# Kernel optimization log

Measured on AMD Instinct MI355X. Metric: run time of the kernel, lower is better.

## Reference

```python
import jax, jax.numpy as jnp
import numpy as np

K = 1024
H = 16

def setup_inputs() -> dict:
    key = jax.random.key(0)
    ks = jax.random.split(key, 6)
    s = 1.0 / np.sqrt(K)
    return {
        "x": jax.random.normal(ks[0], (2, 2048, K), dtype=jnp.float32),
        "Wq": jax.random.uniform(ks[1], (K, K), jnp.float32, -s, s),
        "Wk": jax.random.uniform(ks[2], (K, K), jnp.float32, -s, s),
        "Wv": jax.random.uniform(ks[3], (K, K), jnp.float32, -s, s),
        "Wu": jax.random.uniform(ks[4], (K, K), jnp.float32, -s, s),
        "bu": jax.random.uniform(ks[5], (K,), jnp.float32, -s, s),
    }

def reference(x, Wq, Wk, Wv, Wu, bu):
    b, t, k = x.shape
    hd = k // H  # head dim = 64
    scale = jnp.asarray(k, x.dtype) ** 0.25  # Bloem-style: scale q and k each by k^(1/4)
    # nn.Linear(bias=False): y = x @ W.T
    q = (jnp.einsum('btk,ok->bto', x, Wq) / scale).reshape(b, t, H, hd)
    kk = (jnp.einsum('btk,ok->bto', x, Wk) / scale).reshape(b, t, H, hd)
    v = jnp.einsum('btk,ok->bto', x, Wv).reshape(b, t, H, hd)
    dot = jnp.einsum('bthd,bshd->bhts', q, kk)  # [b,h,t,t]
    att = jax.nn.softmax(dot, axis=-1)
    out = jnp.einsum('bhts,bshd->bthd', att, v).reshape(b, t, k)
    return jnp.einsum('btk,ok->bto', out, Wu) + bu
```

## Files before the change

### kernel.cpp

```cpp
#include <hip/hip_runtime.h>

typedef __bf16 bf16;
typedef bf16  bf16x8 __attribute__((ext_vector_type(8)));
typedef bf16  bf16x4 __attribute__((ext_vector_type(4)));
typedef float f32x4  __attribute__((ext_vector_type(4)));

#define MFMA16(a, b, c) __builtin_amdgcn_mfma_f32_16x16x32_bf16((a), (b), (c), 0, 0, 0)
#define AS1 __attribute__((address_space(1)))
#define AS3 __attribute__((address_space(3)))

__device__ __forceinline__ void gld_lds16(const bf16* g, bf16* l) {
    __builtin_amdgcn_global_load_lds((AS1 void*)(g), (AS3 void*)(l), 16, 0, 0);
}


__global__ __launch_bounds__(256) void cvt_x(const float* __restrict__ src, bf16* __restrict__ dst) {
    int idx = (blockIdx.x * 256 + threadIdx.x) * 4;
    float4 v = *(const float4*)(src + idx);
    bf16x4 o;
    o[0] = (bf16)v.x; o[1] = (bf16)v.y; o[2] = (bf16)v.z; o[3] = (bf16)v.w;
    *(bf16x4*)(dst + idx) = o;
}

__global__ __launch_bounds__(256) void cvt_weights(const float* __restrict__ Wq, const float* __restrict__ Wk,
                                                   const float* __restrict__ Wv, const float* __restrict__ Wu,
                                                   bf16* oq, bf16* ok, bf16* ov, bf16* ou,
                                                   float sq, float sk) {
    const float* src; bf16* dst; float sc;
    switch (blockIdx.y) {
        case 0:  src = Wq; dst = oq; sc = sq;   break;
        case 1:  src = Wk; dst = ok; sc = sk;   break;
        case 2:  src = Wv; dst = ov; sc = 1.0f; break;
        default: src = Wu; dst = ou; sc = 1.0f; break;
    }
    int idx = (blockIdx.x * 256 + threadIdx.x) * 4;
    float4 v = *(const float4*)(src + idx);
    bf16x4 o;
    o[0] = (bf16)(v.x * sc); o[1] = (bf16)(v.y * sc);
    o[2] = (bf16)(v.z * sc); o[3] = (bf16)(v.w * sc);
    *(bf16x4*)(dst + idx) = o;
}

__device__ __forceinline__ void gemm_core(const bf16* __restrict__ A, const bf16* __restrict__ B,
                                          int mBase, int nBase, bf16* As, bf16* Bs,
                                          f32x4 acc[4][4]) {
    const int tid = threadIdx.x;
    const int wave = tid >> 6, lane = tid & 63;
    const int g = lane >> 4, lr = lane & 15;
    const int wm = (wave & 1) << 6, wn = (wave >> 1) << 6;
    const int q = lane >> 2;
    const int cswz = ((lane & 3) ^ ((lane >> 3) & 3)) << 3;
    const int pcs  = (g ^ ((lr >> 1) & 3)) << 3;

    const int rb0 = wave << 4, rb1 = rb0 + 64;
    const bf16* a0 = A + (size_t)(mBase + rb0 + q) * 1024 + cswz;
    const bf16* a1 = A + (size_t)(mBase + rb1 + q) * 1024 + cswz;
    const bf16* b0 = B + (size_t)(nBase + rb0 + q) * 1024 + cswz;
    const bf16* b1 = B + (size_t)(nBase + rb1 + q) * 1024 + cswz;

    for (int k0 = 0; k0 < 1024; k0 += 32) {
        __syncthreads();
        gld_lds16(a0 + k0, As + rb0 * 32);
        gld_lds16(a1 + k0, As + rb1 * 32);
        gld_lds16(b0 + k0, Bs + rb0 * 32);
        gld_lds16(b1 + k0, Bs + rb1 * 32);
        __syncthreads();

        bf16x8 af[4], bfr[4];
#pragma unroll
        for (int i = 0; i < 4; i++)
            af[i] = *(const bf16x8*)&As[(wm + (i << 4) + lr) * 32 + pcs];
#pragma unroll
        for (int j = 0; j < 4; j++)
            bfr[j] = *(const bf16x8*)&Bs[(wn + (j << 4) + lr) * 32 + pcs];
#pragma unroll
        for (int i = 0; i < 4; i++)
#pragma unroll
            for (int j = 0; j < 4; j++)
                acc[i][j] = MFMA16(af[i], bfr[j], acc[i][j]);
    }
}

__global__ __launch_bounds__(256) void gemm_qkv(const bf16* __restrict__ A,
                                                const bf16* __restrict__ Wq, const bf16* __restrict__ Wk,
                                                const bf16* __restrict__ Wv,
                                                bf16* __restrict__ Qo, bf16* __restrict__ Ko,
                                                bf16* __restrict__ Vto) {
    __shared__ bf16 As[128 * 32];
    __shared__ bf16 Bs[128 * 32];
    const int tid = threadIdx.x;
    const int wave = tid >> 6, lane = tid & 63;
    const int g = lane >> 4, lr = lane & 15;
    const int wm = (wave & 1) << 6, wn = (wave >> 1) << 6;
    const int z = blockIdx.z;

    const bf16 *Ap, *Bp;
    int mBase, nBase;
    if (z == 2) { Ap = Wv; Bp = A;            mBase = blockIdx.x * 128; nBase = blockIdx.y * 128; }
    else        { Ap = A;  Bp = z ? Wk : Wq;  mBase = blockIdx.y * 128; nBase = blockIdx.x * 128; }

    f32x4 acc[4][4] = {};
    gemm_core(Ap, Bp, mBase, nBase, As, Bs, acc);

#pragma unroll
    for (int i = 0; i < 4; i++)
#pragma unroll
        for (int j = 0; j < 4; j++)
#pragma unroll
            for (int r = 0; r < 4; r++) {
                int m = mBase + wm + (i << 4) + (g << 2) + r;
                int n = nBase + wn + (j << 4) + lr;
                bf16 v = (bf16)acc[i][j][r];
                if (z == 2) {
                    int h = m >> 6, d = m & 63, b = n >> 11, t = n & 2047;
                    Vto[((size_t)(((b << 4) + h) << 6) + d) * 2048 + t] = v;
                } else {
                    int b = m >> 11, t = m & 2047, h = n >> 6, d = n & 63;
                    bf16* dst = (z == 0) ? Qo : Ko;
                    dst[(((size_t)((b << 4) + h) * 2048 + t) << 6) + d] = v;
                }
            }
}

__global__ __launch_bounds__(256) void gemm_out(const bf16* __restrict__ A, const bf16* __restrict__ B,
                                                const float* __restrict__ bias, float* __restrict__ out) {
    __shared__ bf16 As[128 * 32];
    __shared__ bf16 Bs[128 * 32];
    const int tid = threadIdx.x;
    const int wave = tid >> 6, lane = tid & 63;
    const int g = lane >> 4, lr = lane & 15;
    const int wm = (wave & 1) << 6, wn = (wave >> 1) << 6;
    const int mBase = blockIdx.y * 128, nBase = blockIdx.x * 128;

    f32x4 acc[4][4] = {};
    gemm_core(A, B, mBase, nBase, As, Bs, acc);

#pragma unroll
    for (int i = 0; i < 4; i++)
#pragma unroll
        for (int j = 0; j < 4; j++) {
            int n = nBase + wn + (j << 4) + lr;
            float bv = bias[n];
#pragma unroll
            for (int r = 0; r < 4; r++) {
                int m = mBase + wm + (i << 4) + (g << 2) + r;
                out[((size_t)m << 10) + n] = acc[i][j][r] + bv;
            }
        }
}

__global__ __launch_bounds__(256) void attn(const bf16* __restrict__ Q, const bf16* __restrict__ Kt,
                                            const bf16* __restrict__ Vt, bf16* __restrict__ O) {
    __shared__ bf16 Qs[2][128][32];
    __shared__ bf16 Ks[2][128][32];
    __shared__ bf16 Vs[4][64][32];
    bf16 (*Ps)[32][32] = (bf16(*)[32][32]) & Qs[0][0][0];

    const int tid = threadIdx.x;
    const int wave = tid >> 6, lane = tid & 63;
    const int g = lane >> 4, lr = lane & 15;
    const int q = lane >> 2;
    const int cswz = ((lane & 3) ^ ((lane >> 3) & 3)) << 3;
    const int pcs  = (g ^ ((lr >> 1) & 3)) << 3;
    const int pw0 = ((((g >> 1))     ^ ((lr >> 1) & 3)) << 3) + ((g & 1) << 2);
    const int pw1 = (((2 + (g >> 1)) ^ ((lr >> 1) & 3)) << 3) + ((g & 1) << 2);

    const int bh = blockIdx.y;
    const int qBase = blockIdx.x << 7;

    const bf16* Qg = Q + ((size_t)bh * 2048 + qBase) * 64;
    const bf16* Kg = Kt + (size_t)bh * 2048 * 64;
    const bf16* Vg = Vt + (size_t)bh * 64 * 2048;

#pragma unroll
    for (int i = 0; i < 4; i++) {
        int bi = (wave << 2) + i;
        int p = bi >> 3, rb = (bi & 7) << 4;
        gld_lds16(Qg + (rb + q) * 64 + (p << 5) + cswz, &Qs[p][rb][0]);
    }
    __syncthreads();

    bf16x8 qf[2][2];
#pragma unroll
    for (int ks = 0; ks < 2; ks++)
#pragma unroll
        for (int tt = 0; tt < 2; tt++)
            qf[ks][tt] = *(const bf16x8*)&Qs[ks][(wave << 5) + (tt << 4) + lr][pcs];

    f32x4 oacc[2][4] = {};
    float lsum[2] = {0.f, 0.f};

    for (int s0 = 0; s0 < 2048; s0 += 128) {
        __syncthreads();
#pragma unroll
        for (int i = 0; i < 4; i++) {
            int bi = (wave << 2) + i;
            {
                int p = bi >> 3, rb = (bi & 7) << 4;
                gld_lds16(Kg + (size_t)(s0 + rb + q) * 64 + (p << 5) + cswz, &Ks[p][rb][0]);
            }
            {
                int p = bi >> 2, rb = (bi & 3) << 4;
                gld_lds16(Vg + (size_t)(rb + q) * 2048 + s0 + (p << 5) + cswz, &Vs[p][rb][0]);
            }
        }
        __syncthreads();

#pragma unroll
        for (int ks2 = 0; ks2 < 4; ks2++) {
            f32x4 sacc[2][2] = {};
#pragma unroll
            for (int isub = 0; isub < 2; isub++) {
                int is = (ks2 << 1) + isub;
#pragma unroll
                for (int ks = 0; ks < 2; ks++) {
                    bf16x8 kf = *(const bf16x8*)&Ks[ks][(is << 4) + lr][pcs];
                    sacc[isub][0] = MFMA16(kf, qf[ks][0], sacc[isub][0]);
                    sacc[isub][1] = MFMA16(kf, qf[ks][1], sacc[isub][1]);
                }
            }
#pragma unroll
            for (int isub = 0; isub < 2; isub++)
#pragma unroll
                for (int tt = 0; tt < 2; tt++) {
                    f32x4 s = sacc[isub][tt];
                    float e0 = __builtin_amdgcn_exp2f(s[0]);
                    float e1 = __builtin_amdgcn_exp2f(s[1]);
                    float e2 = __builtin_amdgcn_exp2f(s[2]);
                    float e3 = __builtin_amdgcn_exp2f(s[3]);
                    lsum[tt] += (e0 + e1) + (e2 + e3);
                    bf16x4 pb;
                    pb[0] = (bf16)e0; pb[1] = (bf16)e1; pb[2] = (bf16)e2; pb[3] = (bf16)e3;
                    *(bf16x4*)&Ps[wave][(tt << 4) + lr][isub ? pw1 : pw0] = pb;
                }
            bf16x8 pf0 = *(const bf16x8*)&Ps[wave][lr][pcs];
            bf16x8 pf1 = *(const bf16x8*)&Ps[wave][16 + lr][pcs];
#pragma unroll
            for (int jd = 0; jd < 4; jd++) {
                bf16x8 vf = *(const bf16x8*)&Vs[ks2][(jd << 4) + lr][pcs];
                oacc[0][jd] = MFMA16(pf0, vf, oacc[0][jd]);
                oacc[1][jd] = MFMA16(pf1, vf, oacc[1][jd]);
            }
        }
    }

#pragma unroll
    for (int tt = 0; tt < 2; tt++) {
        lsum[tt] += __shfl_xor(lsum[tt], 16, 64);
        lsum[tt] += __shfl_xor(lsum[tt], 32, 64);
    }
    float linv[2][4];
#pragma unroll
    for (int tt = 0; tt < 2; tt++)
#pragma unroll
        for (int r = 0; r < 4; r++)
            linv[tt][r] = 1.0f / __shfl(lsum[tt], (g << 2) + r, 64);

    const int b = bh >> 4, h = bh & 15;
#pragma unroll
    for (int tt = 0; tt < 2; tt++)
#pragma unroll
        for (int jd = 0; jd < 4; jd++)
#pragma unroll
            for (int r = 0; r < 4; r++) {
                int t = qBase + (wave << 5) + (tt << 4) + (g << 2) + r;
                int col = (h << 6) + (jd << 4) + lr;
                O[(((size_t)(b * 2048 + t)) << 10) + col] = (bf16)(oacc[tt][jd][r] * linv[tt][r]);
            }
}

extern "C" void kernel_launch(void* const* d_in, const int* in_sizes, int n_in,
                              void* d_out, int out_size, void* d_ws, size_t ws_size,
                              hipStream_t stream) {
    const float* x  = (const float*)d_in[0];
    const float* Wq = (const float*)d_in[1];
    const float* Wk = (const float*)d_in[2];
    const float* Wv = (const float*)d_in[3];
    const float* Wu = (const float*)d_in[4];
    const float* bu = (const float*)d_in[5];
    float* out = (float*)d_out;

    char* ws = (char*)d_ws;
    bf16* xbf  = (bf16*)(ws);
    bf16* wqbf = (bf16*)(ws + ((size_t)8  << 20));
    bf16* wkbf = (bf16*)(ws + ((size_t)10 << 20));
    bf16* wvbf = (bf16*)(ws + ((size_t)12 << 20));
    bf16* wubf = (bf16*)(ws + ((size_t)14 << 20));
    bf16* Qb   = (bf16*)(ws + ((size_t)16 << 20));
    bf16* Kb   = (bf16*)(ws + ((size_t)24 << 20));
    bf16* Vtb  = (bf16*)(ws + ((size_t)32 << 20));
    bf16* attnO = xbf;

    const float iscale_k = 0.17677669529663687f;
    const float iscale_q = 0.25503540109f;

    cvt_x<<<4096, 256, 0, stream>>>(x, xbf);
    cvt_weights<<<dim3(1024, 4), 256, 0, stream>>>(Wq, Wk, Wv, Wu, wqbf, wkbf, wvbf, wubf,
                                                   iscale_q, iscale_k);

    gemm_qkv<<<dim3(8, 32, 3), 256, 0, stream>>>(xbf, wqbf, wkbf, wvbf, Qb, Kb, Vtb);
    attn<<<dim3(16, 32), 256, 0, stream>>>(Qb, Kb, Vtb, attnO);
    gemm_out<<<dim3(8, 32), 256, 0, stream>>>(attnO, wubf, bu, out);
}
```

Baseline: 200.4 us.

## Merge conversion kernels, double GEMM K-step, compute softmax row sums via MFMA

The x and weight conversion kernels are merged into one launch, saving one kernel launch. The GEMM core now loads 64-wide K tiles into two 32-wide LDS slabs per sync, which halves the number of barriers per K loop. In attention, the softmax denominator is accumulated by an extra MFMA against a vector of ones instead of scalar adds and cross-lane shuffles. That adds two MFMAs per step and sums the rounded bf16 probabilities, so the normalisation may differ slightly from the fp32 sums.

```diff
diff --git a/kernel.cpp b/kernel.cpp
--- a/kernel.cpp
+++ b/kernel.cpp
@@ -14,26 +14,24 @@
 }
 
 
-__global__ __launch_bounds__(256) void cvt_x(const float* __restrict__ src, bf16* __restrict__ dst) {
-    int idx = (blockIdx.x * 256 + threadIdx.x) * 4;
-    float4 v = *(const float4*)(src + idx);
-    bf16x4 o;
-    o[0] = (bf16)v.x; o[1] = (bf16)v.y; o[2] = (bf16)v.z; o[3] = (bf16)v.w;
-    *(bf16x4*)(dst + idx) = o;
-}
-
-__global__ __launch_bounds__(256) void cvt_weights(const float* __restrict__ Wq, const float* __restrict__ Wk,
-                                                   const float* __restrict__ Wv, const float* __restrict__ Wu,
-                                                   bf16* oq, bf16* ok, bf16* ov, bf16* ou,
-                                                   float sq, float sk) {
-    const float* src; bf16* dst; float sc;
-    switch (blockIdx.y) {
-        case 0:  src = Wq; dst = oq; sc = sq;   break;
-        case 1:  src = Wk; dst = ok; sc = sk;   break;
-        case 2:  src = Wv; dst = ov; sc = 1.0f; break;
-        default: src = Wu; dst = ou; sc = 1.0f; break;
+__global__ __launch_bounds__(256) void cvt_all(const float* __restrict__ x,
+                                               const float* __restrict__ Wq, const float* __restrict__ Wk,
+                                               const float* __restrict__ Wv, const float* __restrict__ Wu,
+                                               bf16* ox, bf16* oq, bf16* ok, bf16* ov, bf16* ou,
+                                               float sq, float sk) {
+    int bid = blockIdx.x;
+    const float* src; bf16* dst; float sc; int base;
+    if (bid < 4096) { src = x; dst = ox; sc = 1.0f; base = bid; }
+    else {
+        int w = (bid - 4096) >> 10; base = (bid - 4096) & 1023;
+        switch (w) {
+            case 0:  src = Wq; dst = oq; sc = sq;   break;
+            case 1:  src = Wk; dst = ok; sc = sk;   break;
+            case 2:  src = Wv; dst = ov; sc = 1.0f; break;
+            default: src = Wu; dst = ou; sc = 1.0f; break;
+        }
     }
-    int idx = (blockIdx.x * 256 + threadIdx.x) * 4;
+    int idx = (base * 256 + threadIdx.x) * 4;
     float4 v = *(const float4*)(src + idx);
     bf16x4 o;
     o[0] = (bf16)(v.x * sc); o[1] = (bf16)(v.y * sc);
@@ -42,7 +40,8 @@
 }
 
 __device__ __forceinline__ void gemm_core(const bf16* __restrict__ A, const bf16* __restrict__ B,
-                                          int mBase, int nBase, bf16* As, bf16* Bs,
+                                          int mBase, int nBase,
+                                          bf16 (*As)[128][32], bf16 (*Bs)[128][32],
                                           f32x4 acc[4][4]) {
     const int tid = threadIdx.x;
     const int wave = tid >> 6, lane = tid & 63;
@@ -52,32 +51,35 @@
     const int cswz = ((lane & 3) ^ ((lane >> 3) & 3)) << 3;
     const int pcs  = (g ^ ((lr >> 1) & 3)) << 3;
 
-    const int rb0 = wave << 4, rb1 = rb0 + 64;
-    const bf16* a0 = A + (size_t)(mBase + rb0 + q) * 1024 + cswz;
-    const bf16* a1 = A + (size_t)(mBase + rb1 + q) * 1024 + cswz;
-    const bf16* b0 = B + (size_t)(nBase + rb0 + q) * 1024 + cswz;
-    const bf16* b1 = B + (size_t)(nBase + rb1 + q) * 1024 + cswz;
-
-    for (int k0 = 0; k0 < 1024; k0 += 32) {
+    const int bi0 = wave << 2;
+
+    for (int k0 = 0; k0 < 1024; k0 += 64) {
         __syncthreads();
-        gld_lds16(a0 + k0, As + rb0 * 32);
-        gld_lds16(a1 + k0, As + rb1 * 32);
-        gld_lds16(b0 + k0, Bs + rb0 * 32);
-        gld_lds16(b1 + k0, Bs + rb1 * 32);
+#pragma unroll
+        for (int i = 0; i < 4; i++) {
+            int bi = bi0 + i;
+            int p = bi >> 3, rb = (bi & 7) << 4;
+            int kof = k0 + (p << 5) + cswz;
+            gld_lds16(A + (size_t)(mBase + rb + q) * 1024 + kof, &As[p][rb][0]);
+            gld_lds16(B + (size_t)(nBase + rb + q) * 1024 + kof, &Bs[p][rb][0]);
+        }
         __syncthreads();
 
-        bf16x8 af[4], bfr[4];
-#pragma unroll
-        for (int i = 0; i < 4; i++)
-            af[i] = *(const bf16x8*)&As[(wm + (i << 4) + lr) * 32 + pcs];
-#pragma unroll
-        for (int j = 0; j < 4; j++)
-            bfr[j] = *(const bf16x8*)&Bs[(wn + (j << 4) + lr) * 32 + pcs];
-#pragma unroll
-        for (int i = 0; i < 4; i++)
+#pragma unroll
+        for (int ks = 0; ks < 2; ks++) {
+            bf16x8 af[4], bfr[4];
+#pragma unroll
+            for (int i = 0; i < 4; i++)
+                af[i] = *(const bf16x8*)&As[ks][wm + (i << 4) + lr][pcs];
 #pragma unroll
             for (int j = 0; j < 4; j++)
-                acc[i][j] = MFMA16(af[i], bfr[j], acc[i][j]);
+                bfr[j] = *(const bf16x8*)&Bs[ks][wn + (j << 4) + lr][pcs];
+#pragma unroll
+            for (int i = 0; i < 4; i++)
+#pragma unroll
+                for (int j = 0; j < 4; j++)
+                    acc[i][j] = MFMA16(af[i], bfr[j], acc[i][j]);
+        }
     }
 }
 
@@ -86,8 +88,8 @@
                                                 const bf16* __restrict__ Wv,
                                                 bf16* __restrict__ Qo, bf16* __restrict__ Ko,
                                                 bf16* __restrict__ Vto) {
-    __shared__ bf16 As[128 * 32];
-    __shared__ bf16 Bs[128 * 32];
+    __shared__ bf16 As[2][128][32];
+    __shared__ bf16 Bs[2][128][32];
     const int tid = threadIdx.x;
     const int wave = tid >> 6, lane = tid & 63;
     const int g = lane >> 4, lr = lane & 15;
@@ -124,8 +126,8 @@
 
 __global__ __launch_bounds__(256) void gemm_out(const bf16* __restrict__ A, const bf16* __restrict__ B,
                                                 const float* __restrict__ bias, float* __restrict__ out) {
-    __shared__ bf16 As[128 * 32];
-    __shared__ bf16 Bs[128 * 32];
+    __shared__ bf16 As[2][128][32];
+    __shared__ bf16 Bs[2][128][32];
     const int tid = threadIdx.x;
     const int wave = tid >> 6, lane = tid & 63;
     const int g = lane >> 4, lr = lane & 15;
@@ -187,8 +189,12 @@
         for (int tt = 0; tt < 2; tt++)
             qf[ks][tt] = *(const bf16x8*)&Qs[ks][(wave << 5) + (tt << 4) + lr][pcs];
 
+    bf16x8 ones;
+#pragma unroll
+    for (int i = 0; i < 8; i++) ones[i] = (bf16)1.0f;
+
     f32x4 oacc[2][4] = {};
-    float lsum[2] = {0.f, 0.f};
+    f32x4 oaccL[2] = {};
 
     for (int s0 = 0; s0 < 2048; s0 += 128) {
         __syncthreads();
@@ -224,13 +230,11 @@
 #pragma unroll
                 for (int tt = 0; tt < 2; tt++) {
                     f32x4 s = sacc[isub][tt];
-                    float e0 = __builtin_amdgcn_exp2f(s[0]);
-                    float e1 = __builtin_amdgcn_exp2f(s[1]);
-                    float e2 = __builtin_amdgcn_exp2f(s[2]);
-                    float e3 = __builtin_amdgcn_exp2f(s[3]);
-                    lsum[tt] += (e0 + e1) + (e2 + e3);
                     bf16x4 pb;
-                    pb[0] = (bf16)e0; pb[1] = (bf16)e1; pb[2] = (bf16)e2; pb[3] = (bf16)e3;
+                    pb[0] = (bf16)__builtin_amdgcn_exp2f(s[0]);
+                    pb[1] = (bf16)__builtin_amdgcn_exp2f(s[1]);
+                    pb[2] = (bf16)__builtin_amdgcn_exp2f(s[2]);
+                    pb[3] = (bf16)__builtin_amdgcn_exp2f(s[3]);
                     *(bf16x4*)&Ps[wave][(tt << 4) + lr][isub ? pw1 : pw0] = pb;
                 }
             bf16x8 pf0 = *(const bf16x8*)&Ps[wave][lr][pcs];
@@ -241,20 +245,17 @@
                 oacc[0][jd] = MFMA16(pf0, vf, oacc[0][jd]);
                 oacc[1][jd] = MFMA16(pf1, vf, oacc[1][jd]);
             }
+            oaccL[0] = MFMA16(pf0, ones, oaccL[0]);
+            oaccL[1] = MFMA16(pf1, ones, oaccL[1]);
         }
     }
 
-#pragma unroll
-    for (int tt = 0; tt < 2; tt++) {
-        lsum[tt] += __shfl_xor(lsum[tt], 16, 64);
-        lsum[tt] += __shfl_xor(lsum[tt], 32, 64);
-    }
     float linv[2][4];
 #pragma unroll
     for (int tt = 0; tt < 2; tt++)
 #pragma unroll
         for (int r = 0; r < 4; r++)
-            linv[tt][r] = 1.0f / __shfl(lsum[tt], (g << 2) + r, 64);
+            linv[tt][r] = 1.0f / oaccL[tt][r];
 
     const int b = bh >> 4, h = bh & 15;
 #pragma unroll
@@ -294,9 +295,8 @@
     const float iscale_k = 0.17677669529663687f;
     const float iscale_q = 0.25503540109f;
 
-    cvt_x<<<4096, 256, 0, stream>>>(x, xbf);
-    cvt_weights<<<dim3(1024, 4), 256, 0, stream>>>(Wq, Wk, Wv, Wu, wqbf, wkbf, wvbf, wubf,
-                                                   iscale_q, iscale_k);
+    cvt_all<<<8192, 256, 0, stream>>>(x, Wq, Wk, Wv, Wu, xbf, wqbf, wkbf, wvbf, wubf,
+                                      iscale_q, iscale_k);
 
     gemm_qkv<<<dim3(8, 32, 3), 256, 0, stream>>>(xbf, wqbf, wkbf, wvbf, Qb, Kb, Vtb);
     attn<<<dim3(16, 32), 256, 0, stream>>>(Qb, Kb, Vtb, attnO);
```

Measured after the change: 205.7 us. 1.03x slower.
